# Optimization experiments

Hardware: AMD Instinct MI355X
Metric: run time of the kernel (lower is better)

## Reference

```python
import jax, jax.numpy as jnp
import numpy as np

EPS = 1e-8

def layernorm(x, g, b):
    mu = jnp.mean(x, axis=-1, keepdims=True)
    var = jnp.mean((x - mu) ** 2, axis=-1, keepdims=True)
    return (x - mu) * jax.lax.rsqrt(var + EPS) * g + b

def setup_inputs() -> dict:
    key = jax.random.key(0)
    ks = jax.random.split(key, 8)
    B, L, H, V = 512, 201, 128, 100001  # V = item_num + 1
    s = 0.02
    return {
        "input_seqs": jax.random.randint(ks[0], (B, L), 0, V),
        "negs": jax.random.randint(ks[1], (B, L), 0, V),
        # item_emb: torch Linear(V, H, bias=False) weight has shape [H, V]
        "emb_W": jax.random.normal(ks[2], (H, V), dtype=jnp.float32) * s,
        # standard GRU cell params (torch GRUCell layout: [3H, H], gate order r,z,n)
        "Wih": jax.random.normal(ks[3], (3 * H, H), dtype=jnp.float32) * s,
        "Whh": jax.random.normal(ks[4], (3 * H, H), dtype=jnp.float32) * s,
        "bih": jnp.zeros((3 * H,), dtype=jnp.float32),
        "bhh": jnp.zeros((3 * H,), dtype=jnp.float32),
        "ln1_g": jnp.ones((H,), dtype=jnp.float32),
        "ln1_b": jnp.zeros((H,), dtype=jnp.float32),
        "ln2_g": jnp.ones((H,), dtype=jnp.float32),
        "ln2_b": jnp.zeros((H,), dtype=jnp.float32),
    }

def gru_seq(x, Wih, Whh, bih, bhh):
    # x: [B, T, H] -> hidden states [B, T, H]
    B, T, H = x.shape
    # precompute input-side gates once (one big GEMM)
    gi = jnp.einsum('bth,gh->btg', x, Wih) + bih  # [B, T, 3H]
    gi = jnp.moveaxis(gi, 1, 0)                    # [T, B, 3H]

    def step(h, gi_t):
        gh = h @ Whh.T + bhh                       # [B, 3H]
        i_r, i_z, i_n = jnp.split(gi_t, 3, axis=-1)
        h_r, h_z, h_n = jnp.split(gh, 3, axis=-1)
        r = jax.nn.sigmoid(i_r + h_r)
        z = jax.nn.sigmoid(i_z + h_z)
        n = jnp.tanh(i_n + r * h_n)
        h_new = (1.0 - z) * n + z * h
        return h_new, h_new

    h0 = jnp.zeros((B, H), dtype=x.dtype)
    _, hs = jax.lax.scan(step, h0, gi)
    return jnp.moveaxis(hs, 0, 1)                  # [B, T, H]

def reference(input_seqs, negs, emb_W, Wih, Whh, bih, bhh, ln1_g, ln1_b, ln2_g, ln2_b):
    seqs = input_seqs[:, :-1]
    pos = input_seqs[:, 1:]
    neg = negs[:, 1:]
    # F.one_hot(idx, V) @ Linear(V,H) weight^T  ==  gather of emb_W columns
    emb = emb_W.T                                  # [V, H]
    seqs_feats = emb[seqs]                         # [B, T, H]
    pos_feats = emb[pos]
    neg_feats = emb[neg]
    # dropout p=0 -> identity
    seqs_feats = layernorm(seqs_feats, ln1_g, ln1_b)
    logits = gru_seq(seqs_feats, Wih, Whh, bih, bhh)
    logits = layernorm(logits, ln2_g, ln2_b)
    pos_logits = jnp.sum(logits * pos_feats, axis=-1)
    neg_logits = jnp.sum(logits * neg_feats, axis=-1)
    return (pos_logits, neg_logits)
```

## Files before the change

### kernel.cpp

```cpp
#include <hip/hip_runtime.h>

typedef unsigned int u32;
typedef unsigned short u16;
typedef __attribute__((ext_vector_type(8))) short bf16x8;
typedef __attribute__((ext_vector_type(4))) float f32x4;

#define B_   512
#define L_   201
#define T_   200
#define H_   128
#define V_   100001
#define G3_  384
#define M_   (B_*T_)
#define GPB  16
#define NBLK (B_/GPB)
#define HS   136

#define OFF_EMBT 256
#define OFF_GI   25600768ull
#define OFF_HSEQ 104243968ull

__device__ __forceinline__ float bf2f(u16 a) {
    return __uint_as_float(((u32)a) << 16);
}
__device__ __forceinline__ void bf2x2(u32 p, float& lo, float& hi) {
    lo = __uint_as_float(p << 16);
    hi = __uint_as_float(p & 0xffff0000u);
}
__device__ __forceinline__ u16 f2bf(float f) {
    u32 u = __float_as_uint(f);
    u32 lsb = (u >> 16) & 1u;
    u += 0x7fffu + lsb;
    return (u16)(u >> 16);
}
__device__ __forceinline__ u32 packbf(float a, float b) {
#if __has_builtin(__builtin_amdgcn_cvt_pk_bf16_f32)
    typedef __attribute__((ext_vector_type(2))) __bf16 bf16x2_t;
    bf16x2_t r = __builtin_amdgcn_cvt_pk_bf16_f32(a, b);
    return *(u32*)&r;
#else
    return (u32)f2bf(a) | ((u32)f2bf(b) << 16);
#endif
}
__device__ __forceinline__ float frcp(float x) {
    return __builtin_amdgcn_rcpf(x);
}
__device__ __forceinline__ float sigmoidf_(float x) {
    return frcp(1.0f + __expf(-x));
}
__device__ __forceinline__ float tanhf_(float x) {
    return 1.0f - 2.0f * frcp(__expf(2.0f * x) + 1.0f);
}
__device__ __forceinline__ void halfred2(float& a, float& b) {
    #pragma unroll
    for (int o = 1; o <= 16; o <<= 1) {
        a += __shfl_xor(a, o, 64);
        b += __shfl_xor(b, o, 64);
    }
}
__device__ __forceinline__ float ldv(const void* p, int dt, int i) {
    return dt ? ((const float*)p)[i] : bf2f(((const u16*)p)[i]);
}
__device__ __forceinline__ void ldsbar() {
    asm volatile("s_waitcnt lgkmcnt(0)\n\ts_barrier" ::: "memory");
}
__device__ __forceinline__ bf16x8 load_frag(const void* W, int dt, int row, int koff) {
    union { bf16x8 v; u32 uu[4]; uint4 q; } r;
    if (dt) {
        const float4* p = (const float4*)((const float*)W + (size_t)row * H_ + koff);
        const float4 a = p[0], b = p[1];
        r.uu[0] = packbf(a.x, a.y); r.uu[1] = packbf(a.z, a.w);
        r.uu[2] = packbf(b.x, b.y); r.uu[3] = packbf(b.z, b.w);
    } else {
        r.q = *(const uint4*)((const u16*)W + (size_t)row * H_ + koff);
    }
    return r.v;
}
#define MFMA16(a, b, c) __builtin_amdgcn_mfma_f32_16x16x32_bf16((a), (b), (c), 0, 0, 0)

__global__ __launch_bounds__(64) void k_sniff(const u32* __restrict__ raw,
                                              int* __restrict__ flag) {
    const int lane = threadIdx.x;
    int big = 0;
    #pragma unroll
    for (int i = 0; i < 16; i++) {
        const u32 w = raw[lane * 16 + i];
        float lo, hi; bf2x2(w, lo, hi);
        if (!(fabsf(lo) <= 16.0f)) big++;
        if (!(fabsf(hi) <= 16.0f)) big++;
    }
    #pragma unroll
    for (int o = 32; o >= 1; o <<= 1) big += __shfl_xor(big, o, 64);
    if (lane == 0) *flag = (big > 8) ? 1 : 0;
}

__global__ __launch_bounds__(1024) void k_transpose(const void* __restrict__ embW,
                                                    u16* __restrict__ embT,
                                                    const int* __restrict__ flag) {
    const int dt = *flag;
    __shared__ u16 tile[32][33];
    const int v0 = blockIdx.x * 32;
    const int h0 = blockIdx.y * 32;
    const int tx = threadIdx.x, ty = threadIdx.y;
    const int v = v0 + tx, h = h0 + ty;
    if (v < V_) {
        u16 val;
        if (dt) val = f2bf(((const float*)embW)[(size_t)h * V_ + v]);
        else    val = ((const u16*)embW)[(size_t)h * V_ + v];
        tile[ty][tx] = val;
    }
    __syncthreads();
    const int vo = v0 + ty, ho = h0 + tx;
    if (vo < V_) embT[(size_t)vo * H_ + ho] = tile[tx][ty];
}

__global__ __launch_bounds__(256) void k_gi(const int* __restrict__ seqs,
                                            const u16* __restrict__ embT,
                                            const void* __restrict__ g1,
                                            const void* __restrict__ b1,
                                            const void* __restrict__ Wih,
                                            const void* __restrict__ bih,
                                            u16* __restrict__ gi2,
                                            const int* __restrict__ flag) {
    const int dt = *flag;
    __shared__ u16 xs[64 * HS];
    const int tid = threadIdx.x;
    const int w = tid >> 6, L = tid & 63;
    const int q = L >> 4, u = L & 15;
    const int lk = L & 31;
    const int hw = w * 2 + (L >> 5);
    const int grp = blockIdx.x / 50;
    const int tc  = blockIdx.x % 50;
    float g1v[4], b1v[4];
    #pragma unroll
    for (int j = 0; j < 4; j++) {
        g1v[j] = ldv(g1, dt, lk * 4 + j);
        b1v[j] = ldv(b1, dt, lk * 4 + j);
    }
    #pragma unroll
    for (int it = 0; it < 8; it++) {
        const int row = hw * 8 + it;
        const int s = row >> 4, bi = row & 15;
        const int b = grp * GPB + bi;
        const int t = tc * 4 + s;
        const int tok = seqs[b * L_ + t];
        const uint2 e = *(const uint2*)&embT[(size_t)tok * H_ + lk * 4];
        float f0, f1, f2, f3; bf2x2(e.x, f0, f1); bf2x2(e.y, f2, f3);
        float s1 = (f0 + f1) + (f2 + f3);
        float s2 = (f0*f0 + f1*f1) + (f2*f2 + f3*f3);
        halfred2(s1, s2);
        const float mu = s1 * (1.0f / H_);
        const float rs = rsqrtf(s2 * (1.0f / H_) - mu * mu + 1e-8f);
        uint2 xw;
        xw.x = packbf((f0-mu)*rs*g1v[0]+b1v[0], (f1-mu)*rs*g1v[1]+b1v[1]);
        xw.y = packbf((f2-mu)*rs*g1v[2]+b1v[2], (f3-mu)*rs*g1v[3]+b1v[3]);
        *(uint2*)&xs[row * HS + lk * 4] = xw;
    }
    bf16x8 af[6][4];
    float bb[6][4];
    #pragma unroll
    for (int j = 0; j < 6; j++) {
        const int nt = w * 6 + j;
        #pragma unroll
        for (int c = 0; c < 4; c++)
            af[j][c] = load_frag(Wih, dt, nt * 16 + u, c * 32 + q * 8);
        if (dt) {
            const float4 bv = *(const float4*)((const float*)bih + nt * 16 + q * 4);
            bb[j][0] = bv.x; bb[j][1] = bv.y; bb[j][2] = bv.z; bb[j][3] = bv.w;
        } else {
            const uint2 bv = *(const uint2*)((const u16*)bih + nt * 16 + q * 4);
            bf2x2(bv.x, bb[j][0], bb[j][1]); bf2x2(bv.y, bb[j][2], bb[j][3]);
        }
    }
    ldsbar();
    #pragma unroll
    for (int s = 0; s < 4; s++) {
        bf16x8 xbv[4];
        #pragma unroll
        for (int c = 0; c < 4; c++)
            xbv[c] = *(const bf16x8*)&xs[(s * 16 + u) * HS + c * 32 + q * 8];
        const int t = tc * 4 + s;
        const size_t base_t = (size_t)(grp * T_ + t) * 6144 + q * 64 + u * 4;
        #pragma unroll
        for (int j = 0; j < 6; j++) {
            const int nt = w * 6 + j;
            f32x4 C = {0.f, 0.f, 0.f, 0.f};
            #pragma unroll
            for (int c = 0; c < 4; c++) C = MFMA16(af[j][c], xbv[c], C);
            uint2 o;
            o.x = packbf(C[0] + bb[j][0], C[1] + bb[j][1]);
            o.y = packbf(C[2] + bb[j][2], C[3] + bb[j][3]);
            *(uint2*)&gi2[base_t + (nt >> 3) * 2048 + (nt & 7) * 256] = o;
        }
    }
}

__global__ __launch_bounds__(512, 2) void k_rec(const u16* __restrict__ gi2,
                                                const void* __restrict__ Whh,
                                                const void* __restrict__ bhh,
                                                u16* __restrict__ hseq2,
                                                const int* __restrict__ flag) {
    const int dt = *flag;
    __shared__ u16 hbuf[2][GPB * HS];
    const int tid = threadIdx.x;
    const int w = tid >> 6, L = tid & 63;
    const int q = L >> 4, u = L & 15;
    const int grp = blockIdx.x;
    for (int i = tid; i < GPB * HS; i += 512) hbuf[0][i] = 0;
    bf16x8 wa[12];
    #pragma unroll
    for (int g = 0; g < 3; g++)
        #pragma unroll
        for (int c = 0; c < 4; c++)
            wa[g * 4 + c] = load_frag(Whh, dt, g * H_ + w * 16 + u, c * 32 + q * 8);
    float sbr[4], sbz[4], bhn[4];
    #pragma unroll
    for (int r = 0; r < 4; r++) {
        const int i = w * 16 + q * 4 + r;
        sbr[r] = ldv(bhh, dt, i);
        sbz[r] = ldv(bhh, dt, H_ + i);
        bhn[r] = ldv(bhh, dt, 2 * H_ + i);
    }
    float hst[4] = {0.f, 0.f, 0.f, 0.f};
    const u16* gp = gi2 + (size_t)grp * T_ * 6144 + (size_t)w * 256 + q * 64 + u * 4;
    u16* hp = hseq2 + (size_t)grp * T_ * 2048 + (size_t)w * 256 + q * 64 + u * 4;
    uint2 gcur[3], gnxt[3];
    #pragma unroll
    for (int g = 0; g < 3; g++) {
        gcur[g] = *(const uint2*)(gp + 0 * 6144 + g * 2048);
        gnxt[g] = *(const uint2*)(gp + 1 * 6144 + g * 2048);
    }
    ldsbar();
    for (int t = 0; t < T_; t++) {
        const int cur = t & 1;
        const int tpre = (t + 2 < T_) ? (t + 2) : (T_ - 1);
        uint2 g2s[3];
        #pragma unroll
        for (int g = 0; g < 3; g++)
            g2s[g] = *(const uint2*)(gp + (size_t)tpre * 6144 + g * 2048);
        bf16x8 hbv[4];
        #pragma unroll
        for (int c = 0; c < 4; c++)
            hbv[c] = *(const bf16x8*)&hbuf[cur][u * HS + c * 32 + q * 8];
        f32x4 z4 = {0.f, 0.f, 0.f, 0.f};
        f32x4 gr0 = z4, gr1 = z4, gz0 = z4, gz1 = z4, gn0 = z4, gn1 = z4;
        gr0 = MFMA16(wa[0], hbv[0], gr0);  gr0 = MFMA16(wa[1], hbv[1], gr0);
        gr1 = MFMA16(wa[2], hbv[2], gr1);  gr1 = MFMA16(wa[3], hbv[3], gr1);
        gz0 = MFMA16(wa[4], hbv[0], gz0);  gz0 = MFMA16(wa[5], hbv[1], gz0);
        gz1 = MFMA16(wa[6], hbv[2], gz1);  gz1 = MFMA16(wa[7], hbv[3], gz1);
        gn0 = MFMA16(wa[8], hbv[0], gn0);  gn0 = MFMA16(wa[9], hbv[1], gn0);
        gn1 = MFMA16(wa[10], hbv[2], gn1); gn1 = MFMA16(wa[11], hbv[3], gn1);
        float gir[4], giz[4], gin[4];
        bf2x2(gcur[0].x, gir[0], gir[1]); bf2x2(gcur[0].y, gir[2], gir[3]);
        bf2x2(gcur[1].x, giz[0], giz[1]); bf2x2(gcur[1].y, giz[2], giz[3]);
        bf2x2(gcur[2].x, gin[0], gin[1]); bf2x2(gcur[2].y, gin[2], gin[3]);
        float hpv[4];
        #pragma unroll
        for (int r = 0; r < 4; r++) {
            const float rr = sigmoidf_(gir[r] + (gr0[r] + gr1[r]) + sbr[r]);
            const float zz = sigmoidf_(giz[r] + (gz0[r] + gz1[r]) + sbz[r]);
            const float nn = tanhf_(gin[r] + rr * ((gn0[r] + gn1[r]) + bhn[r]));
            const float hn = (1.f - zz) * nn + zz * hst[r];
            hst[r] = hn; hpv[r] = hn;
        }
        uint2 hw2;
        hw2.x = packbf(hpv[0], hpv[1]);
        hw2.y = packbf(hpv[2], hpv[3]);
        *(uint2*)&hbuf[cur ^ 1][u * HS + w * 16 + q * 4] = hw2;
        *(uint2*)(hp + (size_t)t * 2048) = hw2;
        gcur[0] = gnxt[0]; gcur[1] = gnxt[1]; gcur[2] = gnxt[2];
        gnxt[0] = g2s[0];  gnxt[1] = g2s[1];  gnxt[2] = g2s[2];
        ldsbar();
    }
}

__global__ __launch_bounds__(256) void k_dot(const int* __restrict__ seqs,
                                             const int* __restrict__ negs,
                                             const u16* __restrict__ hseq2,
                                             const u16* __restrict__ embT,
                                             const void* __restrict__ g2,
                                             const void* __restrict__ b2,
                                             void* __restrict__ out,
                                             const int* __restrict__ flag) {
    const int dt = *flag;
    const int m = blockIdx.x * 4 + (threadIdx.x >> 6);
    const int L = threadIdx.x & 63;
    const int b = m / T_, t = m - b * T_;
    const int grp = b >> 4, bi = b & 15;
    const size_t hoff = (size_t)(grp * T_ + t) * 2048
                      + (size_t)(L >> 3) * 256 + ((L >> 1) & 3) * 64 + bi * 4 + (L & 1) * 2;
    const u32 hh = *(const u32*)&hseq2[hoff];
    float h0, h1; bf2x2(hh, h0, h1);
    float s1 = h0 + h1, s2 = h0 * h0 + h1 * h1;
    #pragma unroll
    for (int o = 1; o <= 32; o <<= 1) {
        s1 += __shfl_xor(s1, o, 64);
        s2 += __shfl_xor(s2, o, 64);
    }
    const float mu = s1 * (1.0f / H_);
    const float rs = rsqrtf(s2 * (1.0f / H_) - mu * mu + 1e-8f);
    float gv0, gv1, bv0, bv1;
    if (dt) {
        const float2 g = ((const float2*)g2)[L];
        const float2 bb = ((const float2*)b2)[L];
        gv0 = g.x; gv1 = g.y; bv0 = bb.x; bv1 = bb.y;
    } else {
        bf2x2(((const u32*)g2)[L], gv0, gv1);
        bf2x2(((const u32*)b2)[L], bv0, bv1);
    }
    const float lo0 = (h0 - mu) * rs * gv0 + bv0;
    const float lo1 = (h1 - mu) * rs * gv1 + bv1;
    const int ptok = seqs[b * L_ + t + 1];
    const int ntok = negs[b * L_ + t + 1];
    const u32 pp = *(const u32*)&embT[(size_t)ptok * H_ + L * 2];
    const u32 nn = *(const u32*)&embT[(size_t)ntok * H_ + L * 2];
    float p0, p1, n0, n1; bf2x2(pp, p0, p1); bf2x2(nn, n0, n1);
    float pe = lo0 * p0 + lo1 * p1;
    float ne = lo0 * n0 + lo1 * n1;
    #pragma unroll
    for (int o = 1; o <= 32; o <<= 1) {
        pe += __shfl_xor(pe, o, 64);
        ne += __shfl_xor(ne, o, 64);
    }
    if (L == 0) {
        if (dt) {
            ((float*)out)[m]      = pe;
            ((float*)out)[M_ + m] = ne;
        } else {
            ((u16*)out)[m]        = f2bf(pe);
            ((u16*)out)[M_ + m]   = f2bf(ne);
        }
    }
}

extern "C" void kernel_launch(void* const* d_in, const int* in_sizes, int n_in,
                              void* d_out, int out_size, void* d_ws, size_t ws_size,
                              hipStream_t stream) {
    const int* seqs = (const int*)d_in[0];
    const int* negs = (const int*)d_in[1];
    const void* embW = d_in[2];
    const void* Wih  = d_in[3];
    const void* Whh  = d_in[4];
    const void* bih  = d_in[5];
    const void* bhh  = d_in[6];
    const void* g1   = d_in[7];
    const void* b1   = d_in[8];
    const void* g2   = d_in[9];
    const void* b2   = d_in[10];

    char* ws = (char*)d_ws;
    int* flag = (int*)ws;
    u16* embT  = (u16*)(ws + OFF_EMBT);
    u16* gi2   = (u16*)(ws + OFF_GI);
    u16* hseq2 = (u16*)(ws + OFF_HSEQ);

    k_sniff<<<1, 64, 0, stream>>>((const u32*)embW, flag);
    k_transpose<<<dim3((V_ + 31) / 32, H_ / 32), dim3(32, 32), 0, stream>>>(embW, embT, flag);
    k_gi<<<M_ / 64, 256, 0, stream>>>(seqs, embT, g1, b1, Wih, bih, gi2, flag);
    k_rec<<<NBLK, 512, 0, stream>>>(gi2, Whh, bhh, hseq2, flag);
    k_dot<<<M_ / 4, 256, 0, stream>>>(seqs, negs, hseq2, embT, g2, b2, d_out, flag);
}
```

Before: 381.2 us.

## Fold GRU hidden biases into MFMA accumulators and remap k_dot to 16 rows per wave

In the recurrent kernel, the hidden-side biases now seed the MFMA accumulators, and the gate math is rewritten with fmaf, which shortens the serial per-step dependency chain. The dot kernel is restructured so each wave handles 16 batch rows for one timestep. Each lane reads contiguous 8-byte chunks of the hseq2 layout and 4-element embedding slices, and reduction needs only two shuffle stages instead of six. This cuts shuffle overhead and gives more coalesced hidden-state reads, at the cost of more registers per lane and scattered 8-byte embedding gathers.

```diff
diff --git a/kernel.cpp b/kernel.cpp
--- a/kernel.cpp
+++ b/kernel.cpp
@@ -49,7 +49,7 @@
     return frcp(1.0f + __expf(-x));
 }
 __device__ __forceinline__ float tanhf_(float x) {
-    return 1.0f - 2.0f * frcp(__expf(2.0f * x) + 1.0f);
+    return fmaf(-2.0f, frcp(__expf(2.0f * x) + 1.0f), 1.0f);
 }
 __device__ __forceinline__ void halfred2(float& a, float& b) {
     #pragma unroll
@@ -213,13 +213,13 @@
         #pragma unroll
         for (int c = 0; c < 4; c++)
             wa[g * 4 + c] = load_frag(Whh, dt, g * H_ + w * 16 + u, c * 32 + q * 8);
-    float sbr[4], sbz[4], bhn[4];
+    f32x4 sbr, sbz, sbn;
     #pragma unroll
     for (int r = 0; r < 4; r++) {
         const int i = w * 16 + q * 4 + r;
         sbr[r] = ldv(bhh, dt, i);
         sbz[r] = ldv(bhh, dt, H_ + i);
-        bhn[r] = ldv(bhh, dt, 2 * H_ + i);
+        sbn[r] = ldv(bhh, dt, 2 * H_ + i);
     }
     float hst[4] = {0.f, 0.f, 0.f, 0.f};
     const u16* gp = gi2 + (size_t)grp * T_ * 6144 + (size_t)w * 256 + q * 64 + u * 4;
@@ -243,7 +243,7 @@
         for (int c = 0; c < 4; c++)
             hbv[c] = *(const bf16x8*)&hbuf[cur][u * HS + c * 32 + q * 8];
         f32x4 z4 = {0.f, 0.f, 0.f, 0.f};
-        f32x4 gr0 = z4, gr1 = z4, gz0 = z4, gz1 = z4, gn0 = z4, gn1 = z4;
+        f32x4 gr0 = sbr, gr1 = z4, gz0 = sbz, gz1 = z4, gn0 = sbn, gn1 = z4;
         gr0 = MFMA16(wa[0], hbv[0], gr0);  gr0 = MFMA16(wa[1], hbv[1], gr0);
         gr1 = MFMA16(wa[2], hbv[2], gr1);  gr1 = MFMA16(wa[3], hbv[3], gr1);
         gz0 = MFMA16(wa[4], hbv[0], gz0);  gz0 = MFMA16(wa[5], hbv[1], gz0);
@@ -257,10 +257,10 @@
         float hpv[4];
         #pragma unroll
         for (int r = 0; r < 4; r++) {
-            const float rr = sigmoidf_(gir[r] + (gr0[r] + gr1[r]) + sbr[r]);
-            const float zz = sigmoidf_(giz[r] + (gz0[r] + gz1[r]) + sbz[r]);
-            const float nn = tanhf_(gin[r] + rr * ((gn0[r] + gn1[r]) + bhn[r]));
-            const float hn = (1.f - zz) * nn + zz * hst[r];
+            const float rr = sigmoidf_(gir[r] + (gr0[r] + gr1[r]));
+            const float zz = sigmoidf_(giz[r] + (gz0[r] + gz1[r]));
+            const float nn = tanhf_(fmaf(rr, gn0[r] + gn1[r], gin[r]));
+            const float hn = fmaf(zz, hst[r] - nn, nn);
             hst[r] = hn; hpv[r] = hn;
         }
         uint2 hw2;
@@ -283,46 +283,65 @@
                                              void* __restrict__ out,
                                              const int* __restrict__ flag) {
     const int dt = *flag;
-    const int m = blockIdx.x * 4 + (threadIdx.x >> 6);
+    const int wid = threadIdx.x >> 6;
     const int L = threadIdx.x & 63;
-    const int b = m / T_, t = m - b * T_;
-    const int grp = b >> 4, bi = b & 15;
-    const size_t hoff = (size_t)(grp * T_ + t) * 2048
-                      + (size_t)(L >> 3) * 256 + ((L >> 1) & 3) * 64 + bi * 4 + (L & 1) * 2;
-    const u32 hh = *(const u32*)&hseq2[hoff];
-    float h0, h1; bf2x2(hh, h0, h1);
-    float s1 = h0 + h1, s2 = h0 * h0 + h1 * h1;
-    #pragma unroll
-    for (int o = 1; o <= 32; o <<= 1) {
-        s1 += __shfl_xor(s1, o, 64);
-        s2 += __shfl_xor(s2, o, 64);
-    }
+    const int q = L >> 4, u = L & 15;
+    const int grp = blockIdx.x / 50;
+    const int t   = (blockIdx.x % 50) * 4 + wid;
+    const int b   = grp * GPB + u;
+    const u16* hc = hseq2 + (size_t)(grp * T_ + t) * 2048;
+    uint2 hv[8];
+    #pragma unroll
+    for (int j = 0; j < 8; j++)
+        hv[j] = *(const uint2*)&hc[j * 256 + L * 4];
+    const int ptok = seqs[b * L_ + t + 1];
+    const int ntok = negs[b * L_ + t + 1];
+    float hf[8][4];
+    float s1 = 0.f, s2 = 0.f;
+    #pragma unroll
+    for (int j = 0; j < 8; j++) {
+        float a0, a1, a2, a3;
+        bf2x2(hv[j].x, a0, a1); bf2x2(hv[j].y, a2, a3);
+        hf[j][0] = a0; hf[j][1] = a1; hf[j][2] = a2; hf[j][3] = a3;
+        s1 += (a0 + a1) + (a2 + a3);
+        s2 += (a0*a0 + a1*a1) + (a2*a2 + a3*a3);
+    }
+    s1 += __shfl_xor(s1, 16, 64); s2 += __shfl_xor(s2, 16, 64);
+    s1 += __shfl_xor(s1, 32, 64); s2 += __shfl_xor(s2, 32, 64);
     const float mu = s1 * (1.0f / H_);
     const float rs = rsqrtf(s2 * (1.0f / H_) - mu * mu + 1e-8f);
-    float gv0, gv1, bv0, bv1;
-    if (dt) {
-        const float2 g = ((const float2*)g2)[L];
-        const float2 bb = ((const float2*)b2)[L];
-        gv0 = g.x; gv1 = g.y; bv0 = bb.x; bv1 = bb.y;
-    } else {
-        bf2x2(((const u32*)g2)[L], gv0, gv1);
-        bf2x2(((const u32*)b2)[L], bv0, bv1);
-    }
-    const float lo0 = (h0 - mu) * rs * gv0 + bv0;
-    const float lo1 = (h1 - mu) * rs * gv1 + bv1;
-    const int ptok = seqs[b * L_ + t + 1];
-    const int ntok = negs[b * L_ + t + 1];
-    const u32 pp = *(const u32*)&embT[(size_t)ptok * H_ + L * 2];
-    const u32 nn = *(const u32*)&embT[(size_t)ntok * H_ + L * 2];
-    float p0, p1, n0, n1; bf2x2(pp, p0, p1); bf2x2(nn, n0, n1);
-    float pe = lo0 * p0 + lo1 * p1;
-    float ne = lo0 * n0 + lo1 * n1;
-    #pragma unroll
-    for (int o = 1; o <= 32; o <<= 1) {
-        pe += __shfl_xor(pe, o, 64);
-        ne += __shfl_xor(ne, o, 64);
-    }
-    if (L == 0) {
+    float pe = 0.f, ne = 0.f;
+    #pragma unroll
+    for (int j = 0; j < 8; j++) {
+        const int io = j * 16 + q * 4;
+        float gv0, gv1, gv2, gv3, bv0, bv1, bv2, bv3;
+        if (dt) {
+            const float4 g = *(const float4*)((const float*)g2 + io);
+            const float4 bbv = *(const float4*)((const float*)b2 + io);
+            gv0 = g.x; gv1 = g.y; gv2 = g.z; gv3 = g.w;
+            bv0 = bbv.x; bv1 = bbv.y; bv2 = bbv.z; bv3 = bbv.w;
+        } else {
+            const uint2 g = *(const uint2*)((const u16*)g2 + io);
+            const uint2 bbv = *(const uint2*)((const u16*)b2 + io);
+            bf2x2(g.x, gv0, gv1); bf2x2(g.y, gv2, gv3);
+            bf2x2(bbv.x, bv0, bv1); bf2x2(bbv.y, bv2, bv3);
+        }
+        const uint2 pp = *(const uint2*)&embT[(size_t)ptok * H_ + io];
+        const uint2 nn = *(const uint2*)&embT[(size_t)ntok * H_ + io];
+        float p0, p1, p2, p3, n0, n1, n2, n3;
+        bf2x2(pp.x, p0, p1); bf2x2(pp.y, p2, p3);
+        bf2x2(nn.x, n0, n1); bf2x2(nn.y, n2, n3);
+        const float lo0 = fmaf((hf[j][0] - mu) * rs, gv0, bv0);
+        const float lo1 = fmaf((hf[j][1] - mu) * rs, gv1, bv1);
+        const float lo2 = fmaf((hf[j][2] - mu) * rs, gv2, bv2);
+        const float lo3 = fmaf((hf[j][3] - mu) * rs, gv3, bv3);
+        pe += (lo0*p0 + lo1*p1) + (lo2*p2 + lo3*p3);
+        ne += (lo0*n0 + lo1*n1) + (lo2*n2 + lo3*n3);
+    }
+    pe += __shfl_xor(pe, 16, 64); ne += __shfl_xor(ne, 16, 64);
+    pe += __shfl_xor(pe, 32, 64); ne += __shfl_xor(ne, 32, 64);
+    if (q == 0) {
+        const int m = b * T_ + t;
         if (dt) {
             ((float*)out)[m]      = pe;
             ((float*)out)[M_ + m] = ne;
@@ -358,5 +377,5 @@
     k_transpose<<<dim3((V_ + 31) / 32, H_ / 32), dim3(32, 32), 0, stream>>>(embW, embT, flag);
     k_gi<<<M_ / 64, 256, 0, stream>>>(seqs, embT, g1, b1, Wih, bih, gi2, flag);
     k_rec<<<NBLK, 512, 0, stream>>>(gi2, Whh, bhh, hseq2, flag);
-    k_dot<<<M_ / 4, 256, 0, stream>>>(seqs, negs, hseq2, embT, g2, b2, d_out, flag);
-}
+    k_dot<<<M_ / 64, 256, 0, stream>>>(seqs, negs, hseq2, embT, g2, b2, d_out, flag);
+}
```

Result: faster. 360.6 us (-5.4%).
